# Kernel optimization log

Hardware: AMD Instinct MI355X
Metric: run time of the kernel (lower is better)

Reference implementation:

```python
import jax, jax.numpy as jnp
from jax import lax
import numpy as np

# dims
B, S, IN, E = 2, 2048, 512, 1024
INNER = 2 * E              # mLSTM up-projection, proj_factor = 2.0
NH = 4                     # mLSTM cell heads
DH = INNER // NH           # 512
QKV_BLK = 4                # qkv_proj_blocksize
NHW = INNER // QKV_BLK     # heads of block-diagonal (headwise) q/k/v projections
K = 4                      # causal conv1d kernel size
EPS = 1e-6                 # mLSTM cell eps
LN_EPS = 1e-5


def setup_inputs() -> dict:
    key = jax.random.key(0)
    ks = jax.random.split(key, 16)
    n = lambda k, shp, s=0.02: jax.random.normal(k, shp, jnp.float32) * s
    z = lambda shp: jnp.zeros(shp, jnp.float32)
    return dict(
        x=jax.random.normal(ks[0], (B, S, IN), jnp.float32),
        w_in=n(ks[1], (IN, E)), b_in=z((E,)),
        ln1_w=jnp.ones((E,), jnp.float32),
        w_up=n(ks[2], (E, 2 * INNER)), b_up=z((2 * INNER,)),
        conv_w=n(ks[3], (INNER, K), 0.1), conv_b=z((INNER,)),
        q_w=n(ks[4], (NHW, QKV_BLK, QKV_BLK), 0.3), q_b=z((INNER,)),
        k_w=n(ks[5], (NHW, QKV_BLK, QKV_BLK), 0.3), k_b=z((INNER,)),
        v_w=n(ks[6], (NHW, QKV_BLK, QKV_BLK), 0.3), v_b=z((INNER,)),
        ig_w=n(ks[7], (3 * INNER, NH)), ig_b=z((NH,)),
        fg_w=n(ks[8], (3 * INNER, NH)), fg_b=jnp.ones((NH,), jnp.float32),
        onorm_w=jnp.ones((INNER,), jnp.float32),
        skip=n(ks[9], (INNER,), 1.0),
        w_down=n(ks[10], (INNER, E)), b_down=z((E,)),
        post_w=jnp.ones((E,), jnp.float32),
    )


def _layernorm(x, w, eps=LN_EPS):
    m = x.mean(-1, keepdims=True)
    v = x.var(-1, keepdims=True)
    return (x - m) / jnp.sqrt(v + eps) * w


def _headwise(x, w, b):
    # block-diagonal linear: x (B,S,INNER) split into NHW blocks of QKV_BLK
    Bx, Sx, _ = x.shape
    y = jnp.einsum('bshd,hod->bsho', x.reshape(Bx, Sx, NHW, QKV_BLK), w)
    return y.reshape(Bx, Sx, INNER) + b


def _mlstm_parallel(q, k, v, ig, fg):
    # q,k,v: (B,NH,S,DH); ig,fg: (B,NH,S). Parallel (stabilized) mLSTM.
    log_f = jax.nn.log_sigmoid(fg)                       # (B,NH,S)
    cum = jnp.cumsum(log_f, axis=-1)                     # inclusive cumsum
    dmat = cum[..., :, None] - cum[..., None, :]         # F_i - F_j  (B,NH,S,S)
    mask = jnp.tril(jnp.ones((S, S), bool))
    logD = jnp.where(mask, dmat + ig[..., None, :], -jnp.inf)
    m = logD.max(-1, keepdims=True)                      # (B,NH,S,1)
    Dm = jnp.exp(logD - m)
    qk = jnp.einsum('bnid,bnjd->bnij', q, k) / jnp.sqrt(jnp.float32(DH))
    C = qk * Dm
    norm = jnp.maximum(jnp.abs(C.sum(-1, keepdims=True)), jnp.exp(-m))
    return jnp.einsum('bnij,bnjd->bnid', C / (norm + EPS), v)


def _forward(x, w_in, b_in, ln1_w, w_up, b_up, conv_w, conv_b,
             q_w, q_b, k_w, k_b, v_w, v_b, ig_w, ig_b, fg_w, fg_b,
             onorm_w, skip, w_down, b_down, post_w):
    h_in = x @ w_in + b_in                               # (B,S,E); dropout = identity (eval)

    # --- mLSTM block: residual + pre-LN ---
    xn = _layernorm(h_in, ln1_w)
    up = xn @ w_up + b_up                                # (B,S,2*INNER)
    x_m, z = jnp.split(up, 2, axis=-1)

    # causal depthwise conv1d + SiLU
    rhs = conv_w.T[:, None, :]                           # (K,1,INNER)
    xc = lax.conv_general_dilated(x_m, rhs, window_strides=(1,),
                                  padding=[(K - 1, 0)],
                                  dimension_numbers=('NHC', 'HIO', 'NHC'),
                                  feature_group_count=INNER) + conv_b
    x_conv_act = jax.nn.silu(xc)

    q = _headwise(x_conv_act, q_w, q_b)                  # (B,S,INNER)
    k = _headwise(x_conv_act, k_w, k_b)
    v = _headwise(x_m, v_w, v_b)

    if_in = jnp.concatenate([q, k, v], axis=-1)          # (B,S,3*INNER)
    ig = (if_in @ ig_w + ig_b).transpose(0, 2, 1)        # (B,NH,S)
    fg = (if_in @ fg_w + fg_b).transpose(0, 2, 1)

    to_heads = lambda t: t.reshape(B, S, NH, DH).transpose(0, 2, 1, 3)
    h = _mlstm_parallel(to_heads(q), to_heads(k), to_heads(v), ig, fg)  # (B,NH,S,DH)

    # multi-head (group) norm over DH, then learned scale over flat features
    hn = (h - h.mean(-1, keepdims=True)) / jnp.sqrt(h.var(-1, keepdims=True) + LN_EPS)
    hn = hn.transpose(0, 2, 1, 3).reshape(B, S, INNER) * onorm_w

    h_skip = hn + skip * x_conv_act                      # learnable skip
    h_gated = h_skip * jax.nn.silu(z)                    # output gate
    y = h_gated @ w_down + b_down                        # (B,S,E)

    out = h_in + y                                       # residual
    return _layernorm(out, post_w)                       # post_blocks_norm


def reference(x, w_in, b_in, ln1_w, w_up, b_up, conv_w, conv_b,
              q_w, q_b, k_w, k_b, v_w, v_b, ig_w, ig_b, fg_w, fg_b,
              onorm_w, skip, w_down, b_down, post_w):
    return _forward(x, w_in, b_in, ln1_w, w_up, b_up, conv_w, conv_b,
                    q_w, q_b, k_w, k_b, v_w, v_b, ig_w, ig_b, fg_w, fg_b,
                    onorm_w, skip, w_down, b_down, post_w)
```

## Files before the change

### kernel.cpp

```cpp
#include <hip/hip_runtime.h>
#include <hip/hip_bf16.h>

typedef __hip_bfloat16 bf16;
typedef float floatx4 __attribute__((ext_vector_type(4)));
typedef short bf16x8 __attribute__((ext_vector_type(8)));

#define B_      2
#define S_      2048
#define IN_     512
#define E_      1024
#define INNER_  2048
#define NH_     4
#define DH_     512
#define T_      (B_*S_)
#define EPS_CELL 1e-6f
#define LN_EPS_  1e-5f
#define LS      72
#define CTB_    4

__device__ inline float b2f(bf16 x){ return __bfloat162float(x); }
__device__ inline bf16  f2b(float x){ return __float2bfloat16(x); }
__device__ inline float u2f(unsigned int u){ union{unsigned int i; float f;} v; v.i = u; return v.f; }
__device__ inline unsigned short f2bu(float x){ bf16 t = __float2bfloat16(x); unsigned short r; __builtin_memcpy(&r,&t,2); return r; }
__device__ inline void unpack8(uint4 u, float* f){
  f[0]=u2f(u.x<<16); f[1]=u2f(u.x&0xffff0000u);
  f[2]=u2f(u.y<<16); f[3]=u2f(u.y&0xffff0000u);
  f[4]=u2f(u.z<<16); f[5]=u2f(u.z&0xffff0000u);
  f[6]=u2f(u.w<<16); f[7]=u2f(u.w&0xffff0000u);
}
__device__ inline uint4 pack8(const float* f){
  uint4 u;
  u.x = (unsigned)f2bu(f[0]) | ((unsigned)f2bu(f[1])<<16);
  u.y = (unsigned)f2bu(f[2]) | ((unsigned)f2bu(f[3])<<16);
  u.z = (unsigned)f2bu(f[4]) | ((unsigned)f2bu(f[5])<<16);
  u.w = (unsigned)f2bu(f[6]) | ((unsigned)f2bu(f[7])<<16);
  return u;
}
__device__ inline void stv(bf16* p, float v){ *p = f2b(v); }
__device__ inline void stv(float* p, float v){ *p = v; }

typedef __attribute__((address_space(3))) unsigned int lds_u32_t;
typedef __attribute__((address_space(1))) const unsigned int glb_u32_t;
__device__ __forceinline__ void cp_async16(const bf16* g, short* l){
  __builtin_amdgcn_global_load_lds((glb_u32_t*)(const void*)g,
                                   (lds_u32_t*)(void*)l, 16, 0, 0);
}
__device__ __forceinline__ int so_(int row, int c8){ return row*64 + (((c8) ^ (row&7))<<3); }
__device__ __forceinline__ int eo_(int row, int ch){ return row*128 + (((ch) ^ (row&15))<<3); }

#define STAGE_ASYNC(dst, srcbase, stride, kk) \
  { int slot_ = (kk)*256 + tid; int r_ = slot_>>3; int c8_ = (slot_&7) ^ (r_&7); \
    cp_async16((srcbase) + (size_t)r_*(stride) + c8_*8, &dst[slot_*8]); }

#define STAGE_ASYNC5(dst, srcbase, stride, kk) \
  { int slot_ = (kk)*512 + tid; int r_ = slot_>>3; int c8_ = (slot_&7) ^ (r_&7); \
    cp_async16((srcbase) + (size_t)r_*(stride) + c8_*8, &dst[slot_*8]); }

__device__ inline void transpose_tile(const float* W, bf16* Wt, int K, int N,
    int n0, int k0, int tid, float (*tl)[65]){
  #pragma unroll
  for (int i=0;i<4;i++){
    int idx = tid + i*256; int r = idx>>4, c4 = idx&15;
    float4 v = *(const float4*)(W + (size_t)(k0+r)*N + n0 + c4*4);
    tl[r][c4*4+0]=v.x; tl[r][c4*4+1]=v.y; tl[r][c4*4+2]=v.z; tl[r][c4*4+3]=v.w;
  }
  __syncthreads();
  #pragma unroll
  for (int i=0;i<4;i++){
    int idx = tid + i*256; int rn = idx>>4, c4 = idx&15;
    ushort4 o;
    o.x=f2bu(tl[c4*4+0][rn]); o.y=f2bu(tl[c4*4+1][rn]);
    o.z=f2bu(tl[c4*4+2][rn]); o.w=f2bu(tl[c4*4+3][rn]);
    *(ushort4*)(Wt + (size_t)(n0+rn)*K + k0 + c4*4) = o;
  }
}

__global__ __launch_bounds__(256) void prep_fused(const float* __restrict__ x,
    const float* __restrict__ w_in, const float* __restrict__ w_up,
    const float* __restrict__ igw, const float* __restrict__ fgw,
    bf16* __restrict__ xbf, bf16* __restrict__ w_in_t, bf16* __restrict__ w_up_t,
    bf16* __restrict__ gwb){
  __shared__ float tl[64][65];
  int bid = blockIdx.x, tid = threadIdx.x;
  if (bid < 1024){
    int i = bid*256 + tid;
    const float4* p = (const float4*)(x) + i*2;
    float4 a = p[0], b = p[1];
    ushort4 o0, o1;
    o0.x=f2bu(a.x); o0.y=f2bu(a.y); o0.z=f2bu(a.z); o0.w=f2bu(a.w);
    o1.x=f2bu(b.x); o1.y=f2bu(b.y); o1.z=f2bu(b.z); o1.w=f2bu(b.w);
    ushort4* q = (ushort4*)(xbf) + i*2;
    q[0]=o0; q[1]=o1;
  } else if (bid < 1152){
    int id = bid - 1024;
    int n0 = (id & 15)*64, k0 = (id >> 4)*64;
    transpose_tile(w_in, w_in_t, IN_, E_, n0, k0, tid, tl);
  } else if (bid < 2176){
    int id = bid - 1152;
    int n0 = (id & 63)*64, k0 = (id >> 6)*64;
    transpose_tile(w_up, w_up_t, E_, 2*INNER_, n0, k0, tid, tl);
  } else {
    int idx = (bid - 2176)*256 + tid;
    if (idx < 3*INNER_){
      int g = idx >> 9;
      int e = (idx >> 6) & 7;
      int l = idx & 63;
      int r = g*512 + l*8 + e;
      float4 a = *(const float4*)(igw + (size_t)r*4);
      float4 b = *(const float4*)(fgw + (size_t)r*4);
      ushort4 o0, o1;
      o0.x=f2bu(a.x); o0.y=f2bu(a.y); o0.z=f2bu(a.z); o0.w=f2bu(a.w);
      o1.x=f2bu(b.x); o1.y=f2bu(b.y); o1.z=f2bu(b.z); o1.w=f2bu(b.w);
      *(ushort4*)(gwb + (size_t)idx*8)     = o0;
      *(ushort4*)(gwb + (size_t)idx*8 + 4) = o1;
    }
  }
}

__global__ __launch_bounds__(256) void mfma_gemm(const bf16* __restrict__ A,
    const bf16* __restrict__ Bt, const float* __restrict__ bias, bf16* __restrict__ C,
    int Kd, int lda, int ldc, int NN){
  int bid = blockIdx.x;
  int MM = gridDim.x / NN;
  int mPerX = MM >> 3;
  int xcd = bid & 7, seq = bid >> 3;
  int nb = seq % NN, mb = xcd*mPerX + seq / NN;
  int n0 = nb*128, m0 = mb*128;
  __shared__ __align__(16) short smem[32768];
  int tid = threadIdx.x;
  int w = tid>>6, l = tid&63, lq = l>>4, lr = l&15;
  int wm = (w>>1)*64, wn = (w&1)*64;
  const bf16* Abase = A + (size_t)m0*lda;
  const bf16* Bbase = Bt + (size_t)n0*Kd;
  floatx4 acc[4][4];
  #pragma unroll
  for (int mi=0;mi<4;mi++){
    #pragma unroll
    for (int ni=0;ni<4;ni++) acc[mi][ni] = (floatx4){0.f,0.f,0.f,0.f};
  }
  short* As0 = smem;          short* Bs0 = smem + 8192;
  short* As1 = smem + 16384;  short* Bs1 = smem + 24576;
  int NT = Kd >> 6;
  #pragma unroll
  for (int kk=0;kk<4;kk++){
    STAGE_ASYNC(As0, Abase, lda, kk);
    STAGE_ASYNC(Bs0, Bbase, Kd, kk);
  }
  __syncthreads();
  for (int t=0; t<NT; ++t){
    short* As  = (t&1) ? As1 : As0;
    short* Bs  = (t&1) ? Bs1 : Bs0;
    short* Asn = (t&1) ? As0 : As1;
    short* Bsn = (t&1) ? Bs0 : Bs1;
    if (t+1 < NT){
      int k0 = (t+1)*64;
      #pragma unroll
      for (int kk=0;kk<4;kk++){
        STAGE_ASYNC(Asn, Abase + k0, lda, kk);
        STAGE_ASYNC(Bsn, Bbase + k0, Kd, kk);
      }
    }
    #pragma unroll
    for (int ks=0; ks<2; ks++){
      bf16x8 af[4], bfr[4];
      #pragma unroll
      for (int mi=0;mi<4;mi++) af[mi] = *(const bf16x8*)&As[so_(wm+mi*16+lr, ks*4+lq)];
      #pragma unroll
      for (int ni=0;ni<4;ni++) bfr[ni] = *(const bf16x8*)&Bs[so_(wn+ni*16+lr, ks*4+lq)];
      #pragma unroll
      for (int mi=0;mi<4;mi++){
        #pragma unroll
        for (int ni=0;ni<4;ni++)
          acc[mi][ni] = __builtin_amdgcn_mfma_f32_16x16x32_bf16(af[mi], bfr[ni], acc[mi][ni], 0,0,0);
      }
    }
    __syncthreads();
  }
  float bb[4];
  #pragma unroll
  for (int ni=0;ni<4;ni++) bb[ni] = bias[n0 + wn + ni*16 + lr];
  #pragma unroll
  for (int mi=0;mi<4;mi++){
    #pragma unroll
    for (int ni=0;ni<4;ni++){
      int coll = wn + ni*16 + lr;
      int ch = coll>>3, off = coll&7;
      #pragma unroll
      for (int r=0;r<4;r++){
        int rowl = wm + mi*16 + lq*4 + r;
        smem[rowl*128 + (((ch) ^ (rowl&15))<<3) + off] = (short)f2bu(acc[mi][ni][r] + bb[ni]);
      }
    }
  }
  __syncthreads();
  #pragma unroll
  for (int i=0;i<8;i++){
    int slot = i*256 + tid;
    int r = slot >> 4, c8 = slot & 15;
    uint4 val = *(const uint4*)&smem[eo_(r, c8)];
    *(uint4*)(C + (size_t)(m0+r)*ldc + n0 + c8*8) = val;
  }
}

__global__ __launch_bounds__(256) void mfma_gemm64(const bf16* __restrict__ A,
    const bf16* __restrict__ Bt, const float* __restrict__ bias, bf16* __restrict__ C,
    int Kd, int lda, int ldc, int NN){
  int bid = blockIdx.x;
  int MM = gridDim.x / NN;
  int mPerX = MM >> 3;
  int xcd = bid & 7, seq = bid >> 3;
  int nb = seq % NN, mb = xcd*mPerX + seq / NN;
  int n0 = nb*128, m0 = mb*64;
  __shared__ __align__(16) short smem[24576];
  int tid = threadIdx.x;
  int w = tid>>6, l = tid&63, lq = l>>4, lr = l&15;
  int wm = (w>>1)*32, wn = (w&1)*64;
  const bf16* Abase = A + (size_t)m0*lda;
  const bf16* Bbase = Bt + (size_t)n0*Kd;
  floatx4 acc[2][4];
  #pragma unroll
  for (int mi=0;mi<2;mi++){
    #pragma unroll
    for (int ni=0;ni<4;ni++) acc[mi][ni] = (floatx4){0.f,0.f,0.f,0.f};
  }
  short* As0 = smem;          short* Bs0 = smem + 4096;
  short* As1 = smem + 12288;  short* Bs1 = smem + 16384;
  int NT = Kd >> 6;
  STAGE_ASYNC(As0, Abase, lda, 0);
  STAGE_ASYNC(As0, Abase, lda, 1);
  #pragma unroll
  for (int kk=0;kk<4;kk++){ STAGE_ASYNC(Bs0, Bbase, Kd, kk); }
  __syncthreads();
  for (int t=0; t<NT; ++t){
    short* As  = (t&1) ? As1 : As0;
    short* Bs  = (t&1) ? Bs1 : Bs0;
    short* Asn = (t&1) ? As0 : As1;
    short* Bsn = (t&1) ? Bs0 : Bs1;
    if (t+1 < NT){
      int k0 = (t+1)*64;
      STAGE_ASYNC(Asn, Abase + k0, lda, 0);
      STAGE_ASYNC(Asn, Abase + k0, lda, 1);
      #pragma unroll
      for (int kk=0;kk<4;kk++){ STAGE_ASYNC(Bsn, Bbase + k0, Kd, kk); }
    }
    #pragma unroll
    for (int ks=0; ks<2; ks++){
      bf16x8 af[2], bfr[4];
      #pragma unroll
      for (int mi=0;mi<2;mi++) af[mi] = *(const bf16x8*)&As[so_(wm+mi*16+lr, ks*4+lq)];
      #pragma unroll
      for (int ni=0;ni<4;ni++) bfr[ni] = *(const bf16x8*)&Bs[so_(wn+ni*16+lr, ks*4+lq)];
      #pragma unroll
      for (int mi=0;mi<2;mi++){
        #pragma unroll
        for (int ni=0;ni<4;ni++)
          acc[mi][ni] = __builtin_amdgcn_mfma_f32_16x16x32_bf16(af[mi], bfr[ni], acc[mi][ni], 0,0,0);
      }
    }
    __syncthreads();
  }
  float bb[4];
  #pragma unroll
  for (int ni=0;ni<4;ni++) bb[ni] = bias[n0 + wn + ni*16 + lr];
  #pragma unroll
  for (int mi=0;mi<2;mi++){
    #pragma unroll
    for (int ni=0;ni<4;ni++){
      int coll = wn + ni*16 + lr;
      int ch = coll>>3, off = coll&7;
      #pragma unroll
      for (int r=0;r<4;r++){
        int rowl = wm + mi*16 + lq*4 + r;
        smem[rowl*128 + (((ch) ^ (rowl&15))<<3) + off] = (short)f2bu(acc[mi][ni][r] + bb[ni]);
      }
    }
  }
  __syncthreads();
  #pragma unroll
  for (int i=0;i<4;i++){
    int slot = i*256 + tid;
    int r = slot >> 4, c8 = slot & 15;
    uint4 val = *(const uint4*)&smem[eo_(r, c8)];
    *(uint4*)(C + (size_t)(m0+r)*ldc + n0 + c8*8) = val;
  }
}

template<typename OutT>
__global__ __launch_bounds__(256) void ln_rows(const bf16* __restrict__ X,
    const bf16* __restrict__ Xadd, const float* __restrict__ w, OutT* __restrict__ Y){
  int row = blockIdx.x, tid = threadIdx.x;
  size_t base = (size_t)row*E_;
  float vals[4], s=0.f, s2=0.f;
  #pragma unroll
  for (int e=0;e<4;e++){
    int c = e*256+tid;
    float v = b2f(X[base+c]);
    if (Xadd) v += b2f(Xadd[base+c]);
    vals[e]=v; s+=v; s2+=v*v;
  }
  __shared__ float sa[256], sb[256];
  sa[tid]=s; sb[tid]=s2; __syncthreads();
  for (int off=128; off>0; off>>=1){
    if (tid<off){ sa[tid]+=sa[tid+off]; sb[tid]+=sb[tid+off]; }
    __syncthreads();
  }
  float mean = sa[0]*(1.f/E_);
  float var  = sb[0]*(1.f/E_) - mean*mean;
  float rstd = rsqrtf(var + LN_EPS_);
  #pragma unroll
  for (int e=0;e<4;e++){
    int c = e*256+tid;
    stv(&Y[base+c], (vals[e]-mean)*rstd*w[c]);
  }
}

__global__ __launch_bounds__(256) void conv_headwise(const bf16* __restrict__ up,
    const float* __restrict__ cw, const float* __restrict__ cb,
    const float* __restrict__ qw, const float* __restrict__ qb,
    const float* __restrict__ kw, const float* __restrict__ kb,
    const float* __restrict__ vw, const float* __restrict__ vb,
    bf16* __restrict__ xca, bf16* __restrict__ q, bf16* __restrict__ k,
    bf16* __restrict__ v){
  int t0 = blockIdx.x*CTB_;
  int s0 = t0 & (S_-1);
  int c0 = threadIdx.x*8;
  int hw0 = c0 >> 2;

  float row[7][8];
  #pragma unroll
  for (int j=0;j<7;j++){
    if (s0-3+j >= 0){
      uint4 rv = *(const uint4*)(up + (size_t)(t0-3+j)*(2*INNER_) + c0);
      unpack8(rv, row[j]);
    } else {
      #pragma unroll
      for (int e=0;e<8;e++) row[j][e]=0.f;
    }
  }

  float xc[CTB_][8];
  {
    float cwv[8][4], cbv[8];
    #pragma unroll
    for (int e=0;e<8;e++){
      float4 w4 = *(const float4*)(cw + (size_t)(c0+e)*4);
      cwv[e][0]=w4.x; cwv[e][1]=w4.y; cwv[e][2]=w4.z; cwv[e][3]=w4.w;
    }
    float4 b0 = *(const float4*)(cb+c0), b1 = *(const float4*)(cb+c0+4);
    cbv[0]=b0.x; cbv[1]=b0.y; cbv[2]=b0.z; cbv[3]=b0.w;
    cbv[4]=b1.x; cbv[5]=b1.y; cbv[6]=b1.z; cbv[7]=b1.w;
    #pragma unroll
    for (int i=0;i<CTB_;i++){
      #pragma unroll
      for (int e=0;e<8;e++){
        float a = cbv[e];
        #pragma unroll
        for (int t=0;t<4;t++) a += row[i+t][e]*cwv[e][t];
        xc[i][e] = a/(1.f+expf(-a));
      }
      *(uint4*)(xca + (size_t)(t0+i)*INNER_ + c0) = pack8(xc[i]);
    }
  }

  {
    float wv_[32], bv[8];
    #pragma unroll
    for (int g=0;g<2;g++){
      #pragma unroll
      for (int r4=0;r4<4;r4++){
        float4 w4 = *(const float4*)(vw + (size_t)(hw0+g)*16 + r4*4);
        wv_[g*16+r4*4+0]=w4.x; wv_[g*16+r4*4+1]=w4.y;
        wv_[g*16+r4*4+2]=w4.z; wv_[g*16+r4*4+3]=w4.w;
      }
    }
    float4 b0 = *(const float4*)(vb+c0), b1 = *(const float4*)(vb+c0+4);
    bv[0]=b0.x; bv[1]=b0.y; bv[2]=b0.z; bv[3]=b0.w;
    bv[4]=b1.x; bv[5]=b1.y; bv[6]=b1.z; bv[7]=b1.w;
    #pragma unroll
    for (int i=0;i<CTB_;i++){
      float ov[8];
      #pragma unroll
      for (int g=0;g<2;g++){
        #pragma unroll
        for (int o=0;o<4;o++){
          float a = bv[g*4+o];
          #pragma unroll
          for (int d=0;d<4;d++) a += row[i+3][g*4+d]*wv_[g*16+o*4+d];
          ov[g*4+o]=a;
        }
      }
      *(uint4*)(v + (size_t)(t0+i)*INNER_ + c0) = pack8(ov);
    }
  }

  {
    float wv_[32], bv[8];
    #pragma unroll
    for (int g=0;g<2;g++){
      #pragma unroll
      for (int r4=0;r4<4;r4++){
        float4 w4 = *(const float4*)(qw + (size_t)(hw0+g)*16 + r4*4);
        wv_[g*16+r4*4+0]=w4.x; wv_[g*16+r4*4+1]=w4.y;
        wv_[g*16+r4*4+2]=w4.z; wv_[g*16+r4*4+3]=w4.w;
      }
    }
    float4 b0 = *(const float4*)(qb+c0), b1 = *(const float4*)(qb+c0+4);
    bv[0]=b0.x; bv[1]=b0.y; bv[2]=b0.z; bv[3]=b0.w;
    bv[4]=b1.x; bv[5]=b1.y; bv[6]=b1.z; bv[7]=b1.w;
    #pragma unroll
    for (int i=0;i<CTB_;i++){
      float ov[8];
      #pragma unroll
      for (int g=0;g<2;g++){
        #pragma unroll
        for (int o=0;o<4;o++){
          float a = bv[g*4+o];
          #pragma unroll
          for (int d=0;d<4;d++) a += xc[i][g*4+d]*wv_[g*16+o*4+d];
          ov[g*4+o]=a;
        }
      }
      *(uint4*)(q + (size_t)(t0+i)*INNER_ + c0) = pack8(ov);
    }
  }

  {
    float wv_[32], bv[8];
    #pragma unroll
    for (int g=0;g<2;g++){
      #pragma unroll
      for (int r4=0;r4<4;r4++){
        float4 w4 = *(const float4*)(kw + (size_t)(hw0+g)*16 + r4*4);
        wv_[g*16+r4*4+0]=w4.x; wv_[g*16+r4*4+1]=w4.y;
        wv_[g*16+r4*4+2]=w4.z; wv_[g*16+r4*4+3]=w4.w;
      }
    }
    float4 b0 = *(const float4*)(kb+c0), b1 = *(const float4*)(kb+c0+4);
    bv[0]=b0.x; bv[1]=b0.y; bv[2]=b0.z; bv[3]=b0.w;
    bv[4]=b1.x; bv[5]=b1.y; bv[6]=b1.z; bv[7]=b1.w;
    #pragma unroll
    for (int i=0;i<CTB_;i++){
      float ov[8];
      #pragma unroll
      for (int g=0;g<2;g++){
        #pragma unroll
        for (int o=0;o<4;o++){
          float a = bv[g*4+o];
          #pragma unroll
          for (int d=0;d<4;d++) a += xc[i][g*4+d]*wv_[g*16+o*4+d];
          ov[g*4+o]=a;
        }
      }
      *(uint4*)(k + (size_t)(t0+i)*INNER_ + c0) = pack8(ov);
    }
  }
}

__global__ __launch_bounds__(256) void gates_transv(const bf16* __restrict__ q,
    const bf16* __restrict__ k, const bf16* __restrict__ v,
    const bf16* __restrict__ gwb, const float* __restrict__ igb,
    const float* __restrict__ fgb, float* __restrict__ igo, float* __restrict__ fgo,
    bf16* __restrict__ vT){
  __shared__ float red[4*32];
  __shared__ short tl[64*LS];
  int bid = blockIdx.x, tid = threadIdx.x;
  if (bid < 512){
    int w = tid >> 6, l = tid & 63;
    int quad = w >> 1, kh = w & 1;
    int tok0 = bid*8 + quad*4;
    float acc[4][8];
    #pragma unroll
    for (int t=0;t<4;t++){
      #pragma unroll
      for (int n=0;n<8;n++) acc[t][n]=0.f;
    }
    #pragma unroll 2
    for (int it=0; it<6; ++it){
      int src = it >> 1, j = it & 1;
      const bf16* sp = (src==0) ? q : ((src==1) ? k : v);
      int pos = kh*1024 + j*512 + l*8;
      int g = src*4 + kh*2 + j;
      uint4 dv[4];
      #pragma unroll
      for (int t=0;t<4;t++)
        dv[t] = *(const uint4*)(sp + (size_t)(tok0+t)*INNER_ + pos);
      float d[4][8];
      #pragma unroll
      for (int t=0;t<4;t++) unpack8(dv[t], d[t]);
      const bf16* wb = gwb + (size_t)g*512*8;
      #pragma unroll
      for (int e=0;e<8;e++){
        uint4 wv = *(const uint4*)(wb + (size_t)(e*64 + l)*8);
        float w8[8]; unpack8(wv, w8);
        #pragma unroll
        for (int t=0;t<4;t++){
          #pragma unroll
          for (int n=0;n<8;n++) acc[t][n] += d[t][e]*w8[n];
        }
      }
    }
    #pragma unroll
    for (int off=1; off<64; off<<=1){
      #pragma unroll
      for (int t=0;t<4;t++){
        #pragma unroll
        for (int n=0;n<8;n++) acc[t][n] += __shfl_xor(acc[t][n], off);
      }
    }
    if (l == 0){
      #pragma unroll
      for (int t=0;t<4;t++){
        #pragma unroll
        for (int n=0;n<8;n++) red[w*32 + t*8 + n] = acc[t][n];
      }
    }
    __syncthreads();
    if (tid < 64){
      int qd = tid >> 5, tn = tid & 31;
      int t = tn >> 3, n = tn & 7;
      float val = red[(qd*2)*32 + tn] + red[(qd*2+1)*32 + tn];
      int tok = bid*8 + qd*4 + t;
      int b = tok >> 11, s = tok & (S_-1);
      if (n < 4) igo[((size_t)(b*NH_+n))*S_ + s] = val + igb[n];
      else       fgo[((size_t)(b*NH_+(n-4)))*S_ + s] = val + fgb[n-4];
    }
  } else {
    int id = bid - 512;
    int sb = id & 31, db = (id >> 5) & 7, h = id >> 8;
    int b = h >> 2, n = h & 3;
    int s0 = sb*64, d0 = db*64;
    #pragma unroll
    for (int i=0;i<2;i++){
      int vv = tid + i*256; int r = vv>>3, c8 = vv&7;
      uint4 x = *(const uint4*)(v + (size_t)(b*S_+s0+r)*INNER_ + n*DH_ + d0 + c8*8);
      *(uint4*)&tl[r*LS + c8*8] = x;
    }
    __syncthreads();
    #pragma unroll
    for (int i=0;i<2;i++){
      int vv = tid + i*256; int r = vv>>3, c8 = vv&7;
      unsigned short tmp[8];
      #pragma unroll
      for (int e=0;e<8;e++) tmp[e] = (unsigned short)tl[(c8*8+e)*LS + r];
      uint4 o; __builtin_memcpy(&o, tmp, 16);
      *(uint4*)(vT + ((size_t)h*DH_ + d0 + r)*S_ + s0 + c8*8) = o;
    }
  }
}

__global__ __launch_bounds__(256) void scan8(const float* __restrict__ igp,
    const float* __restrict__ fgp, float* __restrict__ ap,
    float* __restrict__ Mp, float* __restrict__ flp, float* __restrict__ rowsum){
  int h = blockIdx.x, tid = threadIdx.x;
  const float* fg = fgp + (size_t)h*S_;
  const float* ig = igp + (size_t)h*S_;
  int base = tid*8;
  float loc[8], run = 0.f;
  #pragma unroll
  for (int e=0;e<8;e++){
    float x = fg[base+e];
    float ls = fminf(x,0.f) - log1pf(expf(-fabsf(x)));
    run += ls; loc[e] = run;
  }
  __shared__ float sd[256];
  sd[tid]=run; __syncthreads();
  if (tid==0){ float r=0.f; for(int t=0;t<256;t++){ float t0=sd[t]; sd[t]=r; r+=t0; } }
  __syncthreads();
  float off = sd[tid];
  float lm[8], rm = -3e38f;
  #pragma unroll
  for (int e=0;e<8;e++){
    float F = loc[e]+off; loc[e]=F;
    float aj = ig[base+e]-F;
    ap[(size_t)h*S_+base+e]=aj;
    rm = fmaxf(rm, aj); lm[e]=rm;
  }
  __syncthreads();
  sd[tid]=rm; __syncthreads();
  if (tid==0){ float r=-3e38f; for(int t=0;t<256;t++){ float t0=sd[t]; sd[t]=r; r=fmaxf(r,t0); } }
  __syncthreads();
  float offm = sd[tid];
  #pragma unroll
  for (int e=0;e<8;e++){
    float M = fmaxf(lm[e], offm);
    Mp[(size_t)h*S_+base+e]=M;
    flp[(size_t)h*S_+base+e]=expf(-loc[e]-M);
    rowsum[(size_t)h*S_+base+e]=0.f;
  }
}

__global__ __launch_bounds__(512) void qk_decay_kernel(const bf16* __restrict__ qg,
    const bf16* __restrict__ kg, const float* __restrict__ ap,
    const float* __restrict__ Mp, float* __restrict__ rowsum, bf16* __restrict__ W){
  int h = blockIdx.x & 7;
  int t = 271 - (blockIdx.x >> 3);
  int p = (int)((sqrtf(4.f*t+1.f)-1.f)*0.5f);
  while ((p+1)*(p+2) <= t) p++;
  while (p*(p+1) > t) p--;
  int r0 = t - p*(p+1);
  int nj = p + 1;
  int it = 2*p + (r0 >= nj ? 1 : 0);
  int tj = r0 >= nj ? r0 - nj : r0;
  int b = h >> 2, n = h & 3;
  int i0 = it*64, j0 = tj*128;
  __shared__ __align__(16) short smem[2*12288];
  __shared__ float a_s[128], m_s[64];
  int tid = threadIdx.x;
  if (tid < 128) a_s[tid] = ap[(size_t)h*S_ + j0 + tid];
  if (tid < 64)  m_s[tid] = Mp[(size_t)h*S_ + i0 + tid];
  int w = tid>>6, l = tid&63, lq = l>>4, lr = l&15;
  int wm = (w>>1)*16, wn = (w&1)*64;
  const bf16* Qbase = qg + (size_t)(b*S_+i0)*INNER_ + n*DH_;
  const bf16* Kbase = kg + (size_t)(b*S_+j0)*INNER_ + n*DH_;
  floatx4 acc[4];
  #pragma unroll
  for (int ni=0;ni<4;ni++) acc[ni] = (floatx4){0.f,0.f,0.f,0.f};
  short* Qs0 = smem;          short* Ks0 = smem + 4096;
  short* Qs1 = smem + 12288;  short* Ks1 = smem + 16384;
  STAGE_ASYNC5(Qs0, Qbase, INNER_, 0);
  STAGE_ASYNC5(Ks0, Kbase, INNER_, 0);
  STAGE_ASYNC5(Ks0, Kbase, INNER_, 1);
  __syncthreads();
  const int NT = DH_/64;
  for (int tt=0; tt<NT; ++tt){
    short* Qs  = (tt&1) ? Qs1 : Qs0;
    short* Ks  = (tt&1) ? Ks1 : Ks0;
    short* Qsn = (tt&1) ? Qs0 : Qs1;
    short* Ksn = (tt&1) ? Ks0 : Ks1;
    if (tt+1 < NT){
      int d0 = (tt+1)*64;
      STAGE_ASYNC5(Qsn, Qbase + d0, INNER_, 0);
      STAGE_ASYNC5(Ksn, Kbase + d0, INNER_, 0);
      STAGE_ASYNC5(Ksn, Kbase + d0, INNER_, 1);
    }
    #pragma unroll
    for (int ks=0; ks<2; ks++){
      bf16x8 af, bfr[4];
      af = *(const bf16x8*)&Qs[so_(wm+lr, ks*4+lq)];
      #pragma unroll
      for (int ni=0;ni<4;ni++) bfr[ni] = *(const bf16x8*)&Ks[so_(wn+ni*16+lr, ks*4+lq)];
      #pragma unroll
      for (int ni=0;ni<4;ni++)
        acc[ni] = __builtin_amdgcn_mfma_f32_16x16x32_bf16(af, bfr[ni], acc[ni], 0,0,0);
    }
    __syncthreads();
  }
  const float scale = 0.04419417382415922f;
  float rpart[4];
  #pragma unroll
  for (int r=0;r<4;r++) rpart[r]=0.f;
  #pragma unroll
  for (int ni=0;ni<4;ni++){
    int coll = wn + ni*16 + lr;
    int ch = coll>>3, off = coll&7;
    float av = a_s[coll];
    #pragma unroll
    for (int r=0;r<4;r++){
      int rowl = wm + lq*4 + r;
      int gi = i0 + rowl, gj = j0 + coll;
      float wv = 0.f;
      if (gj <= gi) wv = acc[ni][r]*scale*__expf(av-m_s[rowl]);
      smem[rowl*128 + (((ch) ^ (rowl&15))<<3) + off] = (short)f2bu(wv);
      rpart[r] += wv;
    }
  }
  __syncthreads();
  #pragma unroll
  for (int i=0;i<2;i++){
    int slot = i*512 + tid;
    int r = slot >> 4, c8 = slot & 15;
    uint4 val = *(const uint4*)&smem[eo_(r, c8)];
    *(uint4*)(W + ((size_t)h*S_ + i0 + r)*S_ + j0 + c8*8) = val;
  }
  #pragma unroll
  for (int r=0;r<4;r++){
    float v = rpart[r];
    v += __shfl_xor(v, 1, 16);
    v += __shfl_xor(v, 2, 16);
    v += __shfl_xor(v, 4, 16);
    v += __shfl_xor(v, 8, 16);
    if (lr == 0)
      atomicAdd(&rowsum[(size_t)h*S_ + i0 + wm + lq*4 + r], v);
  }
}

__global__ __launch_bounds__(512) void pv_kernel(const bf16* __restrict__ W,
    const bf16* __restrict__ vT, const float* __restrict__ rowsum,
    const float* __restrict__ fl, bf16* __restrict__ O){
  int h = blockIdx.x & 7;
  int s = blockIdx.x >> 3;
  int ti = 31 - (s >> 2), tn = s & 3;
  int b = h >> 2, n = h & 3;
  int i0 = ti*64, d0 = tn*128;
  __shared__ __align__(16) short smem[2*12288];
  __shared__ float inv_s[64];
  int tid = threadIdx.x;
  if (tid < 64){
    size_t o = (size_t)h*S_ + i0 + tid;
    inv_s[tid] = 1.f/(fmaxf(fabsf(rowsum[o]), fl[o]) + EPS_CELL);
  }
  int w = tid>>6, l = tid&63, lq = l>>4, lr = l&15;
  int wm = (w>>1)*16, wn = (w&1)*64;
  const bf16* Wbase = W + ((size_t)h*S_ + i0)*S_;
  const bf16* Vbase = vT + ((size_t)h*DH_ + d0)*S_;
  floatx4 acc[4];
  #pragma unroll
  for (int ni=0;ni<4;ni++) acc[ni] = (floatx4){0.f,0.f,0.f,0.f};
  short* Ws0 = smem;          short* Vs0 = smem + 4096;
  short* Ws1 = smem + 12288;  short* Vs1 = smem + 16384;
  int NT = (i0 >> 6) + 1;
  STAGE_ASYNC5(Ws0, Wbase, S_, 0);
  STAGE_ASYNC5(Vs0, Vbase, S_, 0);
  STAGE_ASYNC5(Vs0, Vbase, S_, 1);
  __syncthreads();
  for (int tt=0; tt<NT; ++tt){
    short* Ws  = (tt&1) ? Ws1 : Ws0;
    short* Vs  = (tt&1) ? Vs1 : Vs0;
    short* Wsn = (tt&1) ? Ws0 : Ws1;
    short* Vsn = (tt&1) ? Vs0 : Vs1;
    if (tt+1 < NT){
      int j0 = (tt+1)*64;
      STAGE_ASYNC5(Wsn, Wbase + j0, S_, 0);
      STAGE_ASYNC5(Vsn, Vbase + j0, S_, 0);
      STAGE_ASYNC5(Vsn, Vbase + j0, S_, 1);
    }
    #pragma unroll
    for (int ks=0; ks<2; ks++){
      bf16x8 af, bfr[4];
      af = *(const bf16x8*)&Ws[so_(wm+lr, ks*4+lq)];
      #pragma unroll
      for (int ni=0;ni<4;ni++) bfr[ni] = *(const bf16x8*)&Vs[so_(wn+ni*16+lr, ks*4+lq)];
      #pragma unroll
      for (int ni=0;ni<4;ni++)
        acc[ni] = __builtin_amdgcn_mfma_f32_16x16x32_bf16(af, bfr[ni], acc[ni], 0,0,0);
    }
    __syncthreads();
  }
  #pragma unroll
  for (int ni=0;ni<4;ni++){
    int dl = wn + ni*16 + lr;
    int ch = dl>>3, off = dl&7;
    #pragma unroll
    for (int r=0;r<4;r++){
      int rowl = wm + lq*4 + r;
      smem[rowl*128 + (((ch) ^ (rowl&15))<<3) + off] = (short)f2bu(acc[ni][r] * inv_s[rowl]);
    }
  }
  __syncthreads();
  #pragma unroll
  for (int i=0;i<2;i++){
    int slot = i*512 + tid;
    int r = slot >> 4, c8 = slot & 15;
    uint4 val = *(const uint4*)&smem[eo_(r, c8)];
    *(uint4*)(O + (size_t)(b*S_ + i0 + r)*INNER_ + n*DH_ + d0 + c8*8) = val;
  }
}

__global__ __launch_bounds__(256) void headnorm_wdown(const bf16* __restrict__ h,
    const float* __restrict__ onw, const float* __restrict__ skip,
    const bf16* __restrict__ xca, bf16* __restrict__ up,
    const float* __restrict__ w_down, bf16* __restrict__ w_down_t){
  __shared__ float sa[256], sb[256];
  __shared__ float tl[64][65];
  int bid = blockIdx.x, tid = threadIdx.x;
  if (bid < 512){
    int n0 = (bid & 15)*64, k0 = (bid >> 4)*64;
    transpose_tile(w_down, w_down_t, INNER_, E_, n0, k0, tid, tl);
    return;
  }
  int id = bid - 512;
  int n = id & 3; int bs = id >> 2;
  size_t hbase = (size_t)bs*INNER_ + n*DH_;
  float v0 = b2f(h[hbase+tid]);
  float v1 = b2f(h[hbase+256+tid]);
  sa[tid]=v0+v1; sb[tid]=v0*v0+v1*v1;
  __syncthreads();
  for (int off=128; off>0; off>>=1){
    if (tid<off){ sa[tid]+=sa[tid+off]; sb[tid]+=sb[tid+off]; }
    __syncthreads();
  }
  float mean = sa[0]*(1.f/DH_);
  float var  = sb[0]*(1.f/DH_) - mean*mean;
  float rstd = rsqrtf(var + LN_EPS_);
  #pragma unroll
  for (int e=0;e<2;e++){
    int dl = e*256+tid; int c = n*DH_+dl;
    float hv = e ? v1 : v0;
    float hn = (hv-mean)*rstd*onw[c];
    float hs = hn + skip[c]*b2f(xca[(size_t)bs*INNER_+c]);
    size_t zoff = (size_t)bs*(2*INNER_) + INNER_ + c;
    float zv = b2f(up[zoff]);
    float sz = zv/(1.f+expf(-zv));
    up[zoff] = f2b(hs*sz);
  }
}

extern "C" void kernel_launch(void* const* d_in, const int* in_sizes, int n_in,
                              void* d_out, int out_size, void* d_ws, size_t ws_size,
                              hipStream_t stream) {
  const float* x      = (const float*)d_in[0];
  const float* w_in   = (const float*)d_in[1];
  const float* b_in   = (const float*)d_in[2];
  const float* ln1_w  = (const float*)d_in[3];
  const float* w_up   = (const float*)d_in[4];
  const float* b_up   = (const float*)d_in[5];
  const float* conv_w = (const float*)d_in[6];
  const float* conv_b = (const float*)d_in[7];
  const float* q_w    = (const float*)d_in[8];
  const float* q_b    = (const float*)d_in[9];
  const float* k_w    = (const float*)d_in[10];
  const float* k_b    = (const float*)d_in[11];
  const float* v_w    = (const float*)d_in[12];
  const float* v_b    = (const float*)d_in[13];
  const float* ig_w   = (const float*)d_in[14];
  const float* ig_b   = (const float*)d_in[15];
  const float* fg_w   = (const float*)d_in[16];
  const float* fg_b   = (const float*)d_in[17];
  const float* onw    = (const float*)d_in[18];
  const float* skip   = (const float*)d_in[19];
  const float* w_down = (const float*)d_in[20];
  const float* b_down = (const float*)d_in[21];
  const float* post_w = (const float*)d_in[22];

  char* p = (char*)d_ws;
  auto alloc = [&](size_t bytes)->void*{ void* r = p; p += (bytes + 255) & ~(size_t)255; return r; };
  bf16* h_in = (bf16*)alloc((size_t)T_*E_*2);
  bf16* xn   = (bf16*)alloc((size_t)T_*E_*2);
  bf16* up   = (bf16*)alloc((size_t)T_*2*INNER_*2);
  bf16* xca  = (bf16*)alloc((size_t)T_*INNER_*2);
  bf16* qb_  = (bf16*)alloc((size_t)T_*INNER_*2);
  bf16* kb_  = (bf16*)alloc((size_t)T_*INNER_*2);
  bf16* vb_  = (bf16*)alloc((size_t)T_*INNER_*2);
  bf16* hb_  = (bf16*)alloc((size_t)T_*INNER_*2);
  float* igbuf = (float*)alloc((size_t)B_*NH_*S_*4);
  float* fgbuf = (float*)alloc((size_t)B_*NH_*S_*4);
  float* abuf  = (float*)alloc((size_t)B_*NH_*S_*4);
  float* Mbuf  = (float*)alloc((size_t)B_*NH_*S_*4);
  float* flbuf = (float*)alloc((size_t)B_*NH_*S_*4);
  float* rsbuf = (float*)alloc((size_t)B_*NH_*S_*4);
  bf16* gwb  = (bf16*)alloc((size_t)3*INNER_*8*2);
  bf16* Wbuf = (bf16*)alloc((size_t)B_*NH_*S_*S_*2);
  bf16* ybuf = xn;
  bf16* vTb  = hb_;
  bf16* obuf = vb_;
  bf16* xbf    = Wbuf;
  bf16* w_in_t = Wbuf + (size_t)T_*IN_;
  bf16* w_up_t = w_in_t + (size_t)E_*IN_;
  bf16* w_down_t = Wbuf;

  prep_fused<<<2200, 256, 0, stream>>>(x, w_in, w_up, ig_w, fg_w,
      xbf, w_in_t, w_up_t, gwb);
  mfma_gemm64<<<(T_/64)*(E_/128), 256, 0, stream>>>(xbf, w_in_t, b_in, h_in, IN_, IN_, E_, E_/128);
  ln_rows<bf16><<<T_, 256, 0, stream>>>(h_in, nullptr, ln1_w, xn);
  mfma_gemm<<<(T_/128)*((2*INNER_)/128), 256, 0, stream>>>(xn, w_up_t, b_up, up, E_, E_, 2*INNER_, (2*INNER_)/128);
  conv_headwise<<<T_/CTB_, 256, 0, stream>>>(up, conv_w, conv_b,
      q_w, q_b, k_w, k_b, v_w, v_b, xca, qb_, kb_, vb_);
  gates_transv<<<512 + 2048, 256, 0, stream>>>(qb_, kb_, vb_, gwb, ig_b, fg_b,
      igbuf, fgbuf, vTb);
  scan8<<<B_*NH_, 256, 0, stream>>>(igbuf, fgbuf, abuf, Mbuf, flbuf, rsbuf);
  qk_decay_kernel<<<8*272, 512, 0, stream>>>(qb_, kb_, abuf, Mbuf, rsbuf, Wbuf);
  pv_kernel<<<8*128, 512, 0, stream>>>(Wbuf, vTb, rsbuf, flbuf, obuf);
  headnorm_wdown<<<512 + T_*NH_, 256, 0, stream>>>(obuf, onw, skip, xca, up,
      w_down, w_down_t);
  mfma_gemm64<<<(T_/64)*(E_/128), 256, 0, stream>>>(up + INNER_, w_down_t, b_down, ybuf, INNER_, 2*INNER_, E_, E_/128);
  ln_rows<float><<<T_, 256, 0, stream>>>(h_in, ybuf, post_w, (float*)d_out);
}
```

Before: 368.6 us.

## Prefetch two K-tiles ahead in GEMMs with explicit vmcnt waits

Restructures both bf16 MFMA GEMM main loops so async global-to-LDS loads for tile t+2 are issued after compute on tile t. Partial s_waitcnt vmcnt waits replace full __syncthreads drains, so one tile's loads stay in flight while the current tile is consumed. The aim is to hide global memory latency behind MFMA work. In exchange it relies on hand-counted vmcnt values and raw barriers, which is fragile if the compiler reorders memory operations or the load count changes.

```diff
diff --git a/kernel.cpp b/kernel.cpp
--- a/kernel.cpp
+++ b/kernel.cpp
@@ -55,6 +55,11 @@
 #define STAGE_ASYNC5(dst, srcbase, stride, kk) \
   { int slot_ = (kk)*512 + tid; int r_ = slot_>>3; int c8_ = (slot_&7) ^ (r_&7); \
     cp_async16((srcbase) + (size_t)r_*(stride) + c8_*8, &dst[slot_*8]); }
+
+#define VMWAIT8() asm volatile("s_waitcnt vmcnt(8)" ::: "memory")
+#define VMWAIT6() asm volatile("s_waitcnt vmcnt(6)" ::: "memory")
+#define VMWAIT0() asm volatile("s_waitcnt vmcnt(0)" ::: "memory")
+#define RAWBAR()  do { asm volatile("" ::: "memory"); __builtin_amdgcn_s_barrier(); asm volatile("" ::: "memory"); } while(0)
 
 __device__ inline void transpose_tile(const float* W, bf16* Wt, int K, int N,
     int n0, int k0, int tid, float (*tl)[65]){
@@ -146,20 +151,16 @@
     STAGE_ASYNC(As0, Abase, lda, kk);
     STAGE_ASYNC(Bs0, Bbase, Kd, kk);
   }
-  __syncthreads();
+  #pragma unroll
+  for (int kk=0;kk<4;kk++){
+    STAGE_ASYNC(As1, Abase + 64, lda, kk);
+    STAGE_ASYNC(Bs1, Bbase + 64, Kd, kk);
+  }
   for (int t=0; t<NT; ++t){
-    short* As  = (t&1) ? As1 : As0;
-    short* Bs  = (t&1) ? Bs1 : Bs0;
-    short* Asn = (t&1) ? As0 : As1;
-    short* Bsn = (t&1) ? Bs0 : Bs1;
-    if (t+1 < NT){
-      int k0 = (t+1)*64;
-      #pragma unroll
-      for (int kk=0;kk<4;kk++){
-        STAGE_ASYNC(Asn, Abase + k0, lda, kk);
-        STAGE_ASYNC(Bsn, Bbase + k0, Kd, kk);
-      }
-    }
+    if (t < NT-1) { VMWAIT8(); } else { VMWAIT0(); }
+    RAWBAR();
+    short* As = (t&1) ? As1 : As0;
+    short* Bs = (t&1) ? Bs1 : Bs0;
     #pragma unroll
     for (int ks=0; ks<2; ks++){
       bf16x8 af[4], bfr[4];
@@ -174,11 +175,20 @@
           acc[mi][ni] = __builtin_amdgcn_mfma_f32_16x16x32_bf16(af[mi], bfr[ni], acc[mi][ni], 0,0,0);
       }
     }
-    __syncthreads();
+    RAWBAR();
+    if (t+2 < NT){
+      int k0 = (t+2)*64;
+      #pragma unroll
+      for (int kk=0;kk<4;kk++){
+        STAGE_ASYNC(As, Abase + k0, lda, kk);
+        STAGE_ASYNC(Bs, Bbase + k0, Kd, kk);
+      }
+    }
   }
   float bb[4];
   #pragma unroll
   for (int ni=0;ni<4;ni++) bb[ni] = bias[n0 + wn + ni*16 + lr];
+  __syncthreads();
   #pragma unroll
   for (int mi=0;mi<4;mi++){
     #pragma unroll
@@ -230,19 +240,15 @@
   STAGE_ASYNC(As0, Abase, lda, 1);
   #pragma unroll
   for (int kk=0;kk<4;kk++){ STAGE_ASYNC(Bs0, Bbase, Kd, kk); }
-  __syncthreads();
+  STAGE_ASYNC(As1, Abase + 64, lda, 0);
+  STAGE_ASYNC(As1, Abase + 64, lda, 1);
+  #pragma unroll
+  for (int kk=0;kk<4;kk++){ STAGE_ASYNC(Bs1, Bbase + 64, Kd, kk); }
   for (int t=0; t<NT; ++t){
-    short* As  = (t&1) ? As1 : As0;
-    short* Bs  = (t&1) ? Bs1 : Bs0;
-    short* Asn = (t&1) ? As0 : As1;
-    short* Bsn = (t&1) ? Bs0 : Bs1;
-    if (t+1 < NT){
-      int k0 = (t+1)*64;
-      STAGE_ASYNC(Asn, Abase + k0, lda, 0);
-      STAGE_ASYNC(Asn, Abase + k0, lda, 1);
-      #pragma unroll
-      for (int kk=0;kk<4;kk++){ STAGE_ASYNC(Bsn, Bbase + k0, Kd, kk); }
-    }
+    if (t < NT-1) { VMWAIT6(); } else { VMWAIT0(); }
+    RAWBAR();
+    short* As = (t&1) ? As1 : As0;
+    short* Bs = (t&1) ? Bs1 : Bs0;
     #pragma unroll
     for (int ks=0; ks<2; ks++){
       bf16x8 af[2], bfr[4];
@@ -257,11 +263,19 @@
           acc[mi][ni] = __builtin_amdgcn_mfma_f32_16x16x32_bf16(af[mi], bfr[ni], acc[mi][ni], 0,0,0);
       }
     }
-    __syncthreads();
+    RAWBAR();
+    if (t+2 < NT){
+      int k0 = (t+2)*64;
+      STAGE_ASYNC(As, Abase + k0, lda, 0);
+      STAGE_ASYNC(As, Abase + k0, lda, 1);
+      #pragma unroll
+      for (int kk=0;kk<4;kk++){ STAGE_ASYNC(Bs, Bbase + k0, Kd, kk); }
+    }
   }
   float bb[4];
   #pragma unroll
   for (int ni=0;ni<4;ni++) bb[ni] = bias[n0 + wn + ni*16 + lr];
+  __syncthreads();
   #pragma unroll
   for (int mi=0;mi<2;mi++){
     #pragma unroll
```

Result: faster. 357.4 us (median of 2 runs) (-3.0%).
